# Performance work log

Hardware: AMD Instinct MI355X
Metric: run time of the kernel (lower is better)

The kernel has to match this reference:

```python
import jax, jax.numpy as jnp
import numpy as np


def setup_inputs() -> dict:
    key = jax.random.key(0)
    k1, k2, k3, k4, k5 = jax.random.split(key, 5)
    B, ENS, XDIM, YDIM = 8, 256, 8192, 256
    return {
        "Ens_ten": jax.random.normal(k1, (B, ENS, XDIM), dtype=jnp.float32),
        "H": jax.random.normal(k2, (XDIM, YDIM), dtype=jnp.float32),
        "y_true_mean": jax.random.normal(k3, (1, YDIM), dtype=jnp.float32),
        "y_true_std": jax.random.normal(k4, (1, YDIM), dtype=jnp.float32),
        "noise": jax.random.normal(k5, (B, YDIM, ENS), dtype=jnp.float32),
    }


def reference(Ens_ten, H, y_true_mean, y_true_std, noise):
    # Ens_ten: [b, ens, xdim]; H: [xdim, ydim]
    b, ens, xdim = Ens_ten.shape
    Y = jnp.einsum('bex,xy->bey', Ens_ten, H)          # observation_func (linear)
    x_m = jnp.mean(Ens_ten, axis=1, keepdims=True)     # [b,1,xdim]
    y_m = jnp.mean(Y, axis=1, keepdims=True)           # [b,1,ydim]
    Xc = jnp.swapaxes(Ens_ten - x_m, 1, 2)             # [b,xdim,ens]
    Yc = jnp.swapaxes(Y - y_m, 1, 2)                   # [b,ydim,ens]
    C_xy = jnp.einsum('bxe,bye->bxy', Xc, Yc) / ens    # [b,xdim,ydim]
    C_yy = jnp.einsum('bue,bve->buv', Yc, Yc) / ens    # [b,ydim,ydim]
    R = jnp.diag(jnp.square(y_true_std)[0])            # [ydim,ydim], broadcasts over batch
    A = R + C_yy                                       # [b,ydim,ydim]
    # torch.linalg.solve(A, C_xy, left=False): K = C_xy @ inv(A)
    K = jnp.swapaxes(
        jnp.linalg.solve(jnp.swapaxes(A, 1, 2), jnp.swapaxes(C_xy, 1, 2)), 1, 2
    )                                                  # [b,xdim,ydim]
    R_2 = noise * jnp.square(y_true_std)[:, :, None]   # [b,ydim,ens]
    innov = y_true_mean[:, :, None] - Yc + R_2         # [b,ydim,ens]
    update = jnp.einsum('bxy,bye->bxe', K, innov)      # [b,xdim,ens]
    return Ens_ten + jnp.swapaxes(update, 1, 2)
```

## Files before the change

### kernel.cpp

```cpp
#include <hip/hip_runtime.h>

#define ENSN 256
#define XDIM 8192
#define YD 256
#define BATCH 8

#define OFF_Y   0
#define OFF_YC  524288
#define OFF_AUG 1048576
#define OFF_W   2097152
#define OFF_XM  2621440

typedef __attribute__((ext_vector_type(4))) short short4v;
typedef __attribute__((ext_vector_type(8))) short short8v;
typedef __attribute__((ext_vector_type(4))) float float4v;

__device__ __forceinline__ unsigned short f2bf_rne(float x) {
    unsigned u = __float_as_uint(x);
    u += 0x7FFFu + ((u >> 16) & 1u);
    return (unsigned short)(u >> 16);
}

__global__ __launch_bounds__(256) void k1_colmean(const float* __restrict__ E,
                                                  float* __restrict__ xm) {
    int x = blockIdx.x * 256 + threadIdx.x;
    int b = blockIdx.y;
    const float* p = E + (size_t)b * ENSN * XDIM + x;
    float s = 0.f;
    #pragma unroll 8
    for (int e = 0; e < ENSN; e++) s += p[(size_t)e * XDIM];
    xm[b * XDIM + x] = s * (1.0f / ENSN);
}

__global__ __launch_bounds__(256) void kc_h(const float* __restrict__ H,
                                            short* __restrict__ Hthi,
                                            short* __restrict__ Htlo) {
    __shared__ float T[64][65];
    int k0 = blockIdx.x * 64, n0 = blockIdx.y * 64;
    int tid = threadIdx.x;
    int c = tid & 63, g = tid >> 6;
    #pragma unroll
    for (int p = 0; p < 16; p++)
        T[g + p * 4][c] = H[(size_t)(k0 + g + p * 4) * YD + n0 + c];
    __syncthreads();
    #pragma unroll
    for (int p = 0; p < 16; p++) {
        int nn = g + p * 4;
        float v = T[c][nn];
        unsigned short h = f2bf_rne(v);
        float hf = __uint_as_float(((unsigned)h) << 16);
        unsigned short l2 = f2bf_rne(v - hf);
        Hthi[(size_t)(n0 + nn) * XDIM + k0 + c] = (short)h;
        Htlo[(size_t)(n0 + nn) * XDIM + k0 + c] = (short)l2;
    }
}

#define EST 40
#define BST 40

__global__ __launch_bounds__(512, 2) void k2m_ygemm(const float* __restrict__ E,
                                                    const short* __restrict__ Hthi,
                                                    const short* __restrict__ Htlo,
                                                    float* __restrict__ Y) {
    __shared__ __align__(16) short Ehi[64 * EST];
    __shared__ __align__(16) short Elo[64 * EST];
    __shared__ __align__(16) short Bhi[256 * BST];
    __shared__ __align__(16) short Blo[256 * BST];
    int tid = threadIdx.x;
    int lane = tid & 63;
    int w = tid >> 6;
    int m0 = blockIdx.x * 64;
    int kb0 = blockIdx.y * 512;
    int wr = (w & 1) * 32;
    int wc = (w >> 1) * 64;
    float4v acc[8];
    #pragma unroll
    for (int i = 0; i < 8; i++) acc[i] = (float4v){0.f, 0.f, 0.f, 0.f};

    int erow = tid >> 3, ecol = (tid & 7) * 4;
    int brow = tid >> 1, bhalf = (tid & 1) * 16;
    int fr = lane & 15, fg = lane >> 4;

    for (int s = 0; s < 16; s++) {
        int kb = kb0 + s * 32;
        float4 ev = *(const float4*)&E[(size_t)(m0 + erow) * XDIM + kb + ecol];
        float vv[4] = {ev.x, ev.y, ev.z, ev.w};
        short4v hi4, lo4;
        #pragma unroll
        for (int j = 0; j < 4; j++) {
            unsigned short h = f2bf_rne(vv[j]);
            float hf = __uint_as_float(((unsigned)h) << 16);
            unsigned short l2 = f2bf_rne(vv[j] - hf);
            hi4[j] = (short)h; lo4[j] = (short)l2;
        }
        *(short4v*)&Ehi[erow * EST + ecol] = hi4;
        *(short4v*)&Elo[erow * EST + ecol] = lo4;
        short8v bh0 = *(const short8v*)&Hthi[(size_t)brow * XDIM + kb + bhalf];
        short8v bh1 = *(const short8v*)&Hthi[(size_t)brow * XDIM + kb + bhalf + 8];
        short8v bl0 = *(const short8v*)&Htlo[(size_t)brow * XDIM + kb + bhalf];
        short8v bl1 = *(const short8v*)&Htlo[(size_t)brow * XDIM + kb + bhalf + 8];
        *(short8v*)&Bhi[brow * BST + bhalf]     = bh0;
        *(short8v*)&Bhi[brow * BST + bhalf + 8] = bh1;
        *(short8v*)&Blo[brow * BST + bhalf]     = bl0;
        *(short8v*)&Blo[brow * BST + bhalf + 8] = bl1;
        __syncthreads();
        short8v ah[2], al[2], bhf[4], blf[4];
        #pragma unroll
        for (int ti = 0; ti < 2; ti++) {
            ah[ti] = *(const short8v*)&Ehi[(wr + ti * 16 + fr) * EST + fg * 8];
            al[ti] = *(const short8v*)&Elo[(wr + ti * 16 + fr) * EST + fg * 8];
        }
        #pragma unroll
        for (int tj = 0; tj < 4; tj++) {
            bhf[tj] = *(const short8v*)&Bhi[(wc + tj * 16 + fr) * BST + fg * 8];
            blf[tj] = *(const short8v*)&Blo[(wc + tj * 16 + fr) * BST + fg * 8];
        }
        #pragma unroll
        for (int ti = 0; ti < 2; ti++)
            #pragma unroll
            for (int tj = 0; tj < 4; tj++) {
                int a = ti * 4 + tj;
                acc[a] = __builtin_amdgcn_mfma_f32_16x16x32_bf16(ah[ti], bhf[tj], acc[a], 0, 0, 0);
                acc[a] = __builtin_amdgcn_mfma_f32_16x16x32_bf16(ah[ti], blf[tj], acc[a], 0, 0, 0);
                acc[a] = __builtin_amdgcn_mfma_f32_16x16x32_bf16(al[ti], bhf[tj], acc[a], 0, 0, 0);
            }
        __syncthreads();
    }
    #pragma unroll
    for (int ti = 0; ti < 2; ti++)
        #pragma unroll
        for (int tj = 0; tj < 4; tj++)
            #pragma unroll
            for (int q = 0; q < 4; q++) {
                int row = m0 + wr + ti * 16 + fg * 4 + q;
                int col = wc + tj * 16 + fr;
                atomicAdd(&Y[row * YD + col], acc[ti * 4 + tj][q]);
            }
}

__global__ __launch_bounds__(256) void k3_center(const float* __restrict__ Y,
                                                 const float* __restrict__ ytm,
                                                 const float* __restrict__ ystd,
                                                 const float* __restrict__ noise,
                                                 float* __restrict__ Yc,
                                                 float* __restrict__ aug) {
    int b = blockIdx.y, tid = threadIdx.x;
    int y0 = blockIdx.x * 64;
    __shared__ float red[4][64];
    __shared__ float ym[64], tms[64], s2[64];
    __shared__ float T[64][65];
    int yl = tid & 63, q = tid >> 6;
    float s = 0.f;
    for (int e = q * 64; e < q * 64 + 64; e++)
        s += Y[(size_t)(b * ENSN + e) * YD + y0 + yl];
    red[q][yl] = s;
    __syncthreads();
    if (tid < 64) {
        ym[tid] = (red[0][tid] + red[1][tid] + red[2][tid] + red[3][tid]) * (1.0f / ENSN);
        float sd = ystd[y0 + tid];
        s2[tid] = sd * sd;
        tms[tid] = ytm[y0 + tid];
    }
    __syncthreads();
    for (int e0 = 0; e0 < ENSN; e0 += 64) {
        #pragma unroll
        for (int p = 0; p < 16; p++) {
            int er = q + p * 4;
            T[er][yl] = Y[(size_t)(b * ENSN + e0 + er) * YD + y0 + yl];
        }
        __syncthreads();
        int ec = yl;
        #pragma unroll
        for (int p = 0; p < 16; p++) {
            int yr = q + p * 4;
            int y = y0 + yr, e = e0 + ec;
            float yv = T[ec][yr] - ym[yr];
            Yc[(size_t)b * YD * ENSN + (size_t)y * ENSN + e] = yv;
            aug[(size_t)b * YD * 512 + (size_t)y * 512 + 256 + e] =
                tms[yr] - yv + noise[(size_t)b * YD * ENSN + (size_t)y * ENSN + e] * s2[yr];
        }
        __syncthreads();
    }
}

__global__ __launch_bounds__(256) void k4_cyy(const float* __restrict__ Yc,
                                              const float* __restrict__ ystd,
                                              float* __restrict__ aug) {
    __shared__ float As[16][68];
    __shared__ float Bs[16][68];
    int tid = threadIdx.x;
    int m0 = blockIdx.x * 64, n0 = blockIdx.y * 64, b = blockIdx.z;
    const float* Ycb = Yc + (size_t)b * YD * ENSN;
    int tr = tid >> 4, tc = tid & 15;
    float acc[4][4];
    #pragma unroll
    for (int i = 0; i < 4; i++)
        #pragma unroll
        for (int j = 0; j < 4; j++) acc[i][j] = 0.f;
    int al = tid & 15, am0 = tid >> 4;
    for (int k0 = 0; k0 < ENSN; k0 += 16) {
        #pragma unroll
        for (int p = 0; p < 4; p++) {
            int am = am0 + p * 16;
            As[al][am] = Ycb[(m0 + am) * ENSN + k0 + al];
            Bs[al][am] = Ycb[(n0 + am) * ENSN + k0 + al];
        }
        __syncthreads();
        #pragma unroll
        for (int kk = 0; kk < 16; kk++) {
            float4 a = *(const float4*)&As[kk][tr * 4];
            float4 bb = *(const float4*)&Bs[kk][tc * 4];
            float af[4] = {a.x, a.y, a.z, a.w};
            float bf[4] = {bb.x, bb.y, bb.z, bb.w};
            #pragma unroll
            for (int i = 0; i < 4; i++)
                #pragma unroll
                for (int j = 0; j < 4; j++) acc[i][j] += af[i] * bf[j];
        }
        __syncthreads();
    }
    float* augb = aug + (size_t)b * YD * 512;
    #pragma unroll
    for (int i = 0; i < 4; i++) {
        int u = m0 + tr * 4 + i;
        #pragma unroll
        for (int j = 0; j < 4; j++) {
            int v = n0 + tc * 4 + j;
            float val = acc[i][j] * (1.0f / ENSN);
            if (u == v) { float sv = ystd[u]; val += sv * sv; }
            augb[u * 512 + v] = val;
        }
    }
}

#define RSTP 484
#define LSTP 233

__global__ __launch_bounds__(1024, 4) void k5p_panel(float* __restrict__ aug, int c0) {
    __shared__ __align__(16) float R[32 * RSTP];
    __shared__ float Ls[32 * LSTP];
    __shared__ __align__(16) float Dg[32 * 33];
    __shared__ float invd[32];
    int b = blockIdx.x, tid = threadIdx.x;
    float* A = aug + (size_t)b * 256 * 512;
    int r5 = tid >> 5, c5 = tid & 31;
    int WR = 480 - c0;
    int W2 = 224 - c0;

    Dg[r5 * 33 + c5] = A[(c0 + r5) * 512 + c0 + c5];
    __syncthreads();
    if (tid < 32) {
        float u[32];
        #pragma unroll
        for (int c = 0; c < 32; c++) u[c] = Dg[tid * 33 + c];
        for (int j = 0; j < 31; j++) {
            float pv = __shfl(u[j], j);
            float f = u[j] / pv;
            #pragma unroll
            for (int c = 0; c < 32; c++) {
                if (c > j) {
                    float ujc = __shfl(u[c], j);
                    if (tid > j) u[c] -= f * ujc;
                }
            }
            if (tid > j) u[j] = f;
        }
        #pragma unroll
        for (int c = 0; c < 32; c++) Dg[tid * 33 + c] = u[c];
        invd[tid] = 1.0f / u[tid];
    }
    for (int cc = c5; cc < WR; cc += 32)
        R[r5 * RSTP + cc] = A[(c0 + r5) * 512 + c0 + 32 + cc];
    for (int row = r5; row < W2; row += 32)
        Ls[c5 * LSTP + row] = A[(c0 + 32 + row) * 512 + c0 + c5];
    __syncthreads();
    A[(c0 + r5) * 512 + c0 + c5] = Dg[r5 * 33 + c5];
    if (tid < WR) {
        float y[32];
        #pragma unroll
        for (int j = 0; j < 32; j++) {
            float s = R[j * RSTP + tid];
            #pragma unroll
            for (int m = 0; m < 32; m++)
                if (m < j) s -= Dg[j * 33 + m] * y[m];
            y[j] = s;
        }
        #pragma unroll
        for (int j = 0; j < 32; j++)
            A[(c0 + j) * 512 + c0 + 32 + tid] = y[j];
    }
    if (tid >= 512 && tid < 512 + W2) {
        int row = tid - 512;
        float l[32];
        #pragma unroll
        for (int j = 0; j < 32; j++) {
            float s = Ls[j * LSTP + row];
            #pragma unroll
            for (int m = 0; m < 32; m++)
                if (m < j) s -= l[m] * Dg[m * 33 + j];
            l[j] = s * invd[j];
        }
        #pragma unroll
        for (int j = 0; j < 32; j++)
            Ls[j * LSTP + row] = l[j];
    }
    __syncthreads();
    for (int row = r5; row < W2; row += 32)
        A[(c0 + 32 + row) * 512 + c0 + c5] = Ls[c5 * LSTP + row];
}

__global__ __launch_bounds__(256) void k5t_trail(float* __restrict__ aug, int c0) {
    __shared__ __align__(16) float Lt[32][36];
    __shared__ __align__(16) float Ut[32][36];
    int b = blockIdx.z, tid = threadIdx.x;
    float* A = aug + (size_t)b * 256 * 512;
    int r0  = c0 + 32 + blockIdx.x * 32;
    int cc0 = c0 + 32 + blockIdx.y * 32;
    int lr = tid >> 3, lc = (tid & 7) * 4;
    *(float4*)&Lt[lr][lc] = *(const float4*)&A[(size_t)(r0 + lr) * 512 + c0 + lc];
    *(float4*)&Ut[lr][lc] = *(const float4*)&A[(size_t)(c0 + lr) * 512 + cc0 + lc];
    __syncthreads();
    float* gp = &A[(size_t)(r0 + lr) * 512 + cc0 + lc];
    float4 acc = *(const float4*)gp;
    #pragma unroll
    for (int k = 0; k < 32; k++) {
        float lv = Lt[lr][k];
        float4 uv = *(const float4*)&Ut[k][lc];
        acc.x -= lv * uv.x;
        acc.y -= lv * uv.y;
        acc.z -= lv * uv.z;
        acc.w -= lv * uv.w;
    }
    *(float4*)gp = acc;
}

__global__ __launch_bounds__(64) void k5i_invu(const float* __restrict__ aug,
                                               float* __restrict__ invU) {
    __shared__ float Dg[32 * 33];
    __shared__ float invd[32];
    int p = blockIdx.x, b = blockIdx.y, tid = threadIdx.x;
    const float* A = aug + (size_t)b * 256 * 512;
    int c0 = 32 * p;
    for (int i = tid; i < 1024; i += 64)
        Dg[(i >> 5) * 33 + (i & 31)] = A[(size_t)(c0 + (i >> 5)) * 512 + c0 + (i & 31)];
    __syncthreads();
    if (tid < 32) invd[tid] = 1.0f / Dg[tid * 33 + tid];
    __syncthreads();
    if (tid < 32) {
        int c = tid;
        float x[32];
        #pragma unroll
        for (int j = 31; j >= 0; j--) {
            float s = (j == c) ? 1.0f : 0.0f;
            #pragma unroll
            for (int m = 0; m < 32; m++)
                if (m > j) s -= Dg[j * 33 + m] * x[m];
            x[j] = s * invd[j];
        }
        float* op = invU + (size_t)(b * 8 + p) * 1024;
        #pragma unroll
        for (int j = 0; j < 32; j++) op[j * 32 + c] = x[j];
    }
}

#define ZST  68
#define LBST 36

__global__ __launch_bounds__(512, 2) void k5s_solve(float* __restrict__ aug,
                                                    const float* __restrict__ invU) {
    __shared__ __align__(16) float Zs[256 * ZST];
    __shared__ __align__(16) float Lb[224 * LBST];
    __shared__ __align__(16) float Dg[32 * 33];
    int b = blockIdx.y, tid = threadIdx.x;
    float* A = aug + (size_t)b * 256 * 512;
    int cb = blockIdx.x * 64;
    int c = tid & 63, g = tid >> 6;
    int rr = tid >> 5, cc = tid & 31;

    for (int r = g; r < 256; r += 8)
        Zs[r * ZST + c] = A[r * 512 + 256 + cb + c];

    for (int p = 7; p >= 0; p--) {
        int c0 = 32 * p, na = c0;
        for (int i = tid; i < 1024; i += 512)
            Dg[(i >> 5) * 33 + (i & 31)] = invU[(size_t)(b * 8 + p) * 1024 + i];
        for (int r = rr; r < na; r += 16)
            Lb[r * LBST + cc] = A[r * 512 + c0 + cc];
        __syncthreads();
        float z[32];
        #pragma unroll
        for (int m = 0; m < 32; m++) z[m] = Zs[(c0 + m) * ZST + c];
        float xr[4];
        #pragma unroll
        for (int r4 = 0; r4 < 4; r4++) {
            const float* dr = &Dg[(g * 4 + r4) * 33];
            float s0 = 0.f, s1 = 0.f, s2 = 0.f, s3 = 0.f;
            #pragma unroll
            for (int m = 0; m < 32; m += 4) {
                s0 += dr[m + 0] * z[m + 0];
                s1 += dr[m + 1] * z[m + 1];
                s2 += dr[m + 2] * z[m + 2];
                s3 += dr[m + 3] * z[m + 3];
            }
            xr[r4] = (s0 + s1) + (s2 + s3);
        }
        __syncthreads();
        #pragma unroll
        for (int r4 = 0; r4 < 4; r4++)
            Zs[(c0 + g * 4 + r4) * ZST + c] = xr[r4];
        __syncthreads();
        if (na > 0) {
            float zx[32];
            #pragma unroll
            for (int k = 0; k < 32; k++) zx[k] = Zs[(c0 + k) * ZST + c];
            for (int r = g; r < na; r += 8) {
                const float* lp = &Lb[r * LBST];
                float a0 = 0.f, a1 = 0.f, a2 = 0.f, a3 = 0.f;
                #pragma unroll
                for (int k = 0; k < 32; k += 4) {
                    float4 lv = *(const float4*)(lp + k);
                    a0 += lv.x * zx[k + 0];
                    a1 += lv.y * zx[k + 1];
                    a2 += lv.z * zx[k + 2];
                    a3 += lv.w * zx[k + 3];
                }
                Zs[r * ZST + c] -= (a0 + a1) + (a2 + a3);
            }
        }
        __syncthreads();
    }

    for (int r = g; r < 256; r += 8)
        A[r * 512 + 256 + cb + c] = Zs[r * ZST + c];
}

__global__ __launch_bounds__(256) void k6_w(const float* __restrict__ Yc,
                                            const float* __restrict__ aug,
                                            float* __restrict__ W) {
    __shared__ float As[16][68];
    __shared__ float Bs[16][68];
    int tid = threadIdx.x;
    int m0 = blockIdx.x * 64, n0 = blockIdx.y * 64, b = blockIdx.z;
    const float* Ycb = Yc + (size_t)b * YD * ENSN;
    const float* augb = aug + (size_t)b * YD * 512;
    int tr = tid >> 4, tc = tid & 15;
    float acc[4][4];
    #pragma unroll
    for (int i = 0; i < 4; i++)
        #pragma unroll
        for (int j = 0; j < 4; j++) acc[i][j] = 0.f;
    int c = tid & 63, kr0 = tid >> 6;
    for (int k0 = 0; k0 < YD; k0 += 16) {
        #pragma unroll
        for (int p = 0; p < 4; p++) {
            int kk = kr0 + p * 4;
            As[kk][c] = Ycb[(k0 + kk) * ENSN + m0 + c];
            Bs[kk][c] = augb[(k0 + kk) * 512 + 256 + n0 + c];
        }
        __syncthreads();
        #pragma unroll
        for (int kk = 0; kk < 16; kk++) {
            float4 a = *(const float4*)&As[kk][tr * 4];
            float4 bb = *(const float4*)&Bs[kk][tc * 4];
            float af[4] = {a.x, a.y, a.z, a.w};
            float bf[4] = {bb.x, bb.y, bb.z, bb.w};
            #pragma unroll
            for (int i = 0; i < 4; i++)
                #pragma unroll
                for (int j = 0; j < 4; j++) acc[i][j] += af[i] * bf[j];
        }
        __syncthreads();
    }
    float* Wb = W + (size_t)b * ENSN * ENSN;
    #pragma unroll
    for (int i = 0; i < 4; i++)
        #pragma unroll
        for (int j = 0; j < 4; j++)
            Wb[(m0 + tr * 4 + i) * ENSN + n0 + tc * 4 + j] = acc[i][j] * (1.0f / ENSN);
}

__global__ __launch_bounds__(256) void kw_w(const float* __restrict__ W,
                                            short* __restrict__ Wthi,
                                            short* __restrict__ Wtlo) {
    __shared__ float T[64][65];
    int f0 = blockIdx.x * 64, e0 = blockIdx.y * 64, b = blockIdx.z;
    const float* Wb = W + (size_t)b * ENSN * ENSN;
    int tid = threadIdx.x;
    int c = tid & 63, g = tid >> 6;
    #pragma unroll
    for (int p = 0; p < 16; p++)
        T[g + p * 4][c] = Wb[(size_t)(f0 + g + p * 4) * ENSN + e0 + c];
    __syncthreads();
    #pragma unroll
    for (int p = 0; p < 16; p++) {
        int ee = g + p * 4;
        float v = T[c][ee];
        unsigned short h = f2bf_rne(v);
        float hf = __uint_as_float(((unsigned)h) << 16);
        unsigned short l2 = f2bf_rne(v - hf);
        size_t o = (size_t)b * ENSN * ENSN + (size_t)(e0 + ee) * ENSN + f0 + c;
        Wthi[o] = (short)h;
        Wtlo[o] = (short)l2;
    }
}

#define WST 36
#define XST 36

__global__ __launch_bounds__(512, 2) void k7m_update(const float* __restrict__ E,
                                                     const short* __restrict__ Wthi,
                                                     const short* __restrict__ Wtlo,
                                                     const float* __restrict__ xm,
                                                     float* __restrict__ out) {
    __shared__ __align__(16) short Ahi[256 * WST];
    __shared__ __align__(16) short Alo[256 * WST];
    __shared__ __align__(16) short Bhi[64 * XST];
    __shared__ __align__(16) short Blo[64 * XST];
    __shared__ float xs[64];
    int tid = threadIdx.x;
    int lane = tid & 63;
    int w = tid >> 6;
    int x0 = blockIdx.x * 64;
    int b = blockIdx.y;
    const short* Whb = Wthi + (size_t)b * ENSN * ENSN;
    const short* Wlb = Wtlo + (size_t)b * ENSN * ENSN;
    const float* Eb = E + (size_t)b * ENSN * XDIM;
    if (tid < 64) xs[tid] = xm[b * XDIM + x0 + tid];
    __syncthreads();
    int wr = (w & 3) * 64;
    int wc = (w >> 2) * 32;
    float4v acc[8];
    #pragma unroll
    for (int i = 0; i < 8; i++) acc[i] = (float4v){0.f, 0.f, 0.f, 0.f};
    int fr = lane & 15, fg = lane >> 4;
    int ae = tid >> 2, ach = (tid & 3) * 8;
    int bx = tid & 63, bkq = tid >> 6;

    for (int s = 0; s < 8; s++) {
        int k0 = s * 32;
        #pragma unroll
        for (int h = 0; h < 2; h++) {
            int e = ae + h * 128;
            *(short8v*)&Ahi[e * WST + ach] = *(const short8v*)&Whb[(size_t)e * ENSN + k0 + ach];
            *(short8v*)&Alo[e * WST + ach] = *(const short8v*)&Wlb[(size_t)e * ENSN + k0 + ach];
        }
        short4v hi4, lo4;
        #pragma unroll
        for (int j = 0; j < 4; j++) {
            float v = Eb[(size_t)(k0 + bkq * 4 + j) * XDIM + x0 + bx] - xs[bx];
            unsigned short h = f2bf_rne(v);
            float hf = __uint_as_float(((unsigned)h) << 16);
            unsigned short l2 = f2bf_rne(v - hf);
            hi4[j] = (short)h; lo4[j] = (short)l2;
        }
        *(short4v*)&Bhi[bx * XST + bkq * 4] = hi4;
        *(short4v*)&Blo[bx * XST + bkq * 4] = lo4;
        __syncthreads();
        short8v ah[4], al[4], bhf[2], blf[2];
        #pragma unroll
        for (int ti = 0; ti < 4; ti++) {
            ah[ti] = *(const short8v*)&Ahi[(wr + ti * 16 + fr) * WST + fg * 8];
            al[ti] = *(const short8v*)&Alo[(wr + ti * 16 + fr) * WST + fg * 8];
        }
        #pragma unroll
        for (int tj = 0; tj < 2; tj++) {
            bhf[tj] = *(const short8v*)&Bhi[(wc + tj * 16 + fr) * XST + fg * 8];
            blf[tj] = *(const short8v*)&Blo[(wc + tj * 16 + fr) * XST + fg * 8];
        }
        #pragma unroll
        for (int ti = 0; ti < 4; ti++)
            #pragma unroll
            for (int tj = 0; tj < 2; tj++) {
                int a = ti * 2 + tj;
                acc[a] = __builtin_amdgcn_mfma_f32_16x16x32_bf16(ah[ti], bhf[tj], acc[a], 0, 0, 0);
                acc[a] = __builtin_amdgcn_mfma_f32_16x16x32_bf16(ah[ti], blf[tj], acc[a], 0, 0, 0);
                acc[a] = __builtin_amdgcn_mfma_f32_16x16x32_bf16(al[ti], bhf[tj], acc[a], 0, 0, 0);
            }
        __syncthreads();
    }
    #pragma unroll
    for (int ti = 0; ti < 4; ti++)
        #pragma unroll
        for (int tj = 0; tj < 2; tj++)
            #pragma unroll
            for (int q = 0; q < 4; q++) {
                int e = wr + ti * 16 + fg * 4 + q;
                int x = x0 + wc + tj * 16 + fr;
                size_t idx = (size_t)(b * ENSN + e) * XDIM + x;
                out[idx] = E[idx] + acc[ti * 2 + tj][q];
            }
}

extern "C" void kernel_launch(void* const* d_in, const int* in_sizes, int n_in,
                              void* d_out, int out_size, void* d_ws, size_t ws_size,
                              hipStream_t stream) {
    const float* Ens   = (const float*)d_in[0];
    const float* H     = (const float*)d_in[1];
    const float* ytm   = (const float*)d_in[2];
    const float* ystd  = (const float*)d_in[3];
    const float* noise = (const float*)d_in[4];
    float* out = (float*)d_out;
    float* ws  = (float*)d_ws;

    float* Y   = ws + OFF_Y;
    float* Yc  = ws + OFF_YC;
    float* aug = ws + OFF_AUG;
    float* W   = ws + OFF_W;
    float* xm  = ws + OFF_XM;
    short* Hthi = (short*)(ws + 524288);
    short* Htlo = (short*)(ws + 1572864);
    short* Wthi = (short*)(ws + 0);
    short* Wtlo = (short*)(ws + 262144);
    float* invU = ws + OFF_W;

    hipMemsetAsync(Y, 0, (size_t)2048 * 256 * sizeof(float), stream);

    k1_colmean<<<dim3(XDIM / 256, BATCH), 256, 0, stream>>>(Ens, xm);
    kc_h<<<dim3(XDIM / 64, YD / 64), 256, 0, stream>>>(H, Hthi, Htlo);
    k2m_ygemm<<<dim3(2048 / 64, 16), 512, 0, stream>>>(Ens, Hthi, Htlo, Y);
    k3_center<<<dim3(4, BATCH), 256, 0, stream>>>(Y, ytm, ystd, noise, Yc, aug);
    k4_cyy<<<dim3(4, 4, BATCH), 256, 0, stream>>>(Yc, ystd, aug);
    for (int p = 0; p < 8; p++) {
        k5p_panel<<<dim3(BATCH), 1024, 0, stream>>>(aug, 32 * p);
        if (p < 7)
            k5t_trail<<<dim3(7 - p, 15 - p, BATCH), 256, 0, stream>>>(aug, 32 * p);
    }
    k5i_invu<<<dim3(8, BATCH), 64, 0, stream>>>(aug, invU);
    k5s_solve<<<dim3(4, BATCH), 512, 0, stream>>>(aug, invU);
    k6_w<<<dim3(4, 4, BATCH), 256, 0, stream>>>(Yc, aug, W);
    kw_w<<<dim3(4, 4, BATCH), 256, 0, stream>>>(W, Wthi, Wtlo);
    k7m_update<<<dim3(XDIM / 64, BATCH), 512, 0, stream>>>(Ens, Wthi, Wtlo, xm, out);
}
```

Baseline: 658.8 us.

## Invert panel diagonal blocks inside LU panel kernel and widen solve grid

The panel kernel now explicitly inverts the 32x32 unit-lower and upper diagonal factors. It then applies those inverses as small dense mat-vecs instead of running serial triangular substitutions for the U row-block and L column-block. The inverse of U is written to global memory there, which removes the separate k5i_invu launch. k5s_solve is retiled to 32 columns per block, doubling its grid to get more parallelism, at the cost of extra shared memory in the panel kernel and a serial inversion step on two warps.

```diff
diff --git a/kernel.cpp b/kernel.cpp
--- a/kernel.cpp
+++ b/kernel.cpp
@@ -236,10 +236,13 @@
 #define RSTP 484
 #define LSTP 233
 
-__global__ __launch_bounds__(1024, 4) void k5p_panel(float* __restrict__ aug, int c0) {
+__global__ __launch_bounds__(1024, 4) void k5p_panel(float* __restrict__ aug,
+                                                     float* __restrict__ invU, int c0) {
     __shared__ __align__(16) float R[32 * RSTP];
     __shared__ float Ls[32 * LSTP];
     __shared__ __align__(16) float Dg[32 * 33];
+    __shared__ float iL[32 * 33];
+    __shared__ float iU[32 * 33];
     __shared__ float invd[32];
     int b = blockIdx.x, tid = threadIdx.x;
     float* A = aug + (size_t)b * 256 * 512;
@@ -275,30 +278,72 @@
         Ls[c5 * LSTP + row] = A[(c0 + 32 + row) * 512 + c0 + c5];
     __syncthreads();
     A[(c0 + r5) * 512 + c0 + c5] = Dg[r5 * 33 + c5];
+    if (tid < 32) {
+        int c = tid;
+        float x[32];
+        #pragma unroll
+        for (int j = 0; j < 32; j++) {
+            float s = (j == c) ? 1.0f : 0.0f;
+            #pragma unroll
+            for (int m = 0; m < 32; m++)
+                if (m < j) s -= Dg[j * 33 + m] * x[m];
+            x[j] = s;
+        }
+        #pragma unroll
+        for (int j = 0; j < 32; j++) iL[j * 33 + c] = x[j];
+    } else if (tid < 64) {
+        int c = tid - 32;
+        float x[32];
+        #pragma unroll
+        for (int j = 31; j >= 0; j--) {
+            float s = (j == c) ? 1.0f : 0.0f;
+            #pragma unroll
+            for (int m = 0; m < 32; m++)
+                if (m > j) s -= Dg[j * 33 + m] * x[m];
+            x[j] = s * invd[j];
+        }
+        #pragma unroll
+        for (int j = 0; j < 32; j++) iU[j * 33 + c] = x[j];
+        float* op = invU + (size_t)(b * 8 + (c0 >> 5)) * 1024;
+        #pragma unroll
+        for (int j = 0; j < 32; j++) op[j * 32 + c] = x[j];
+    }
+    __syncthreads();
     if (tid < WR) {
-        float y[32];
+        float rv[32];
+        #pragma unroll
+        for (int m = 0; m < 32; m++) rv[m] = R[m * RSTP + tid];
         #pragma unroll
         for (int j = 0; j < 32; j++) {
-            float s = R[j * RSTP + tid];
-            #pragma unroll
-            for (int m = 0; m < 32; m++)
-                if (m < j) s -= Dg[j * 33 + m] * y[m];
-            y[j] = s;
-        }
-        #pragma unroll
-        for (int j = 0; j < 32; j++)
-            A[(c0 + j) * 512 + c0 + 32 + tid] = y[j];
+            const float* lj = &iL[j * 33];
+            float s0 = 0.f, s1 = 0.f, s2 = 0.f, s3 = 0.f;
+            #pragma unroll
+            for (int m = 0; m < 32; m += 4) {
+                s0 += lj[m + 0] * rv[m + 0];
+                s1 += lj[m + 1] * rv[m + 1];
+                s2 += lj[m + 2] * rv[m + 2];
+                s3 += lj[m + 3] * rv[m + 3];
+            }
+            A[(c0 + j) * 512 + c0 + 32 + tid] = (s0 + s1) + (s2 + s3);
+        }
     }
     if (tid >= 512 && tid < 512 + W2) {
         int row = tid - 512;
+        float av[32];
+        #pragma unroll
+        for (int m = 0; m < 32; m++) av[m] = Ls[m * LSTP + row];
         float l[32];
         #pragma unroll
         for (int j = 0; j < 32; j++) {
-            float s = Ls[j * LSTP + row];
-            #pragma unroll
-            for (int m = 0; m < 32; m++)
-                if (m < j) s -= l[m] * Dg[m * 33 + j];
-            l[j] = s * invd[j];
+            float s0 = 0.f, s1 = 0.f, s2 = 0.f, s3 = 0.f;
+            #pragma unroll
+            for (int m = 0; m < 32; m += 4) {
+                s0 += av[m + 0] * iU[(m + 0) * 33 + j];
+                s1 += av[m + 1] * iU[(m + 1) * 33 + j];
+                s2 += av[m + 2] * iU[(m + 2) * 33 + j];
+                s3 += av[m + 3] * iU[(m + 3) * 33 + j];
+            }
+            l[j] = (s0 + s1) + (s2 + s3);
         }
         #pragma unroll
         for (int j = 0; j < 32; j++)
@@ -334,36 +379,7 @@
     *(float4*)gp = acc;
 }
 
-__global__ __launch_bounds__(64) void k5i_invu(const float* __restrict__ aug,
-                                               float* __restrict__ invU) {
-    __shared__ float Dg[32 * 33];
-    __shared__ float invd[32];
-    int p = blockIdx.x, b = blockIdx.y, tid = threadIdx.x;
-    const float* A = aug + (size_t)b * 256 * 512;
-    int c0 = 32 * p;
-    for (int i = tid; i < 1024; i += 64)
-        Dg[(i >> 5) * 33 + (i & 31)] = A[(size_t)(c0 + (i >> 5)) * 512 + c0 + (i & 31)];
-    __syncthreads();
-    if (tid < 32) invd[tid] = 1.0f / Dg[tid * 33 + tid];
-    __syncthreads();
-    if (tid < 32) {
-        int c = tid;
-        float x[32];
-        #pragma unroll
-        for (int j = 31; j >= 0; j--) {
-            float s = (j == c) ? 1.0f : 0.0f;
-            #pragma unroll
-            for (int m = 0; m < 32; m++)
-                if (m > j) s -= Dg[j * 33 + m] * x[m];
-            x[j] = s * invd[j];
-        }
-        float* op = invU + (size_t)(b * 8 + p) * 1024;
-        #pragma unroll
-        for (int j = 0; j < 32; j++) op[j * 32 + c] = x[j];
-    }
-}
-
-#define ZST  68
+#define ZST  36
 #define LBST 36
 
 __global__ __launch_bounds__(512, 2) void k5s_solve(float* __restrict__ aug,
@@ -373,11 +389,11 @@
     __shared__ __align__(16) float Dg[32 * 33];
     int b = blockIdx.y, tid = threadIdx.x;
     float* A = aug + (size_t)b * 256 * 512;
-    int cb = blockIdx.x * 64;
-    int c = tid & 63, g = tid >> 6;
+    int cb = blockIdx.x * 32;
+    int c = tid & 31, g = tid >> 5;
     int rr = tid >> 5, cc = tid & 31;
 
-    for (int r = g; r < 256; r += 8)
+    for (int r = g; r < 256; r += 16)
         Zs[r * ZST + c] = A[r * 512 + 256 + cb + c];
 
     for (int p = 7; p >= 0; p--) {
@@ -390,10 +406,10 @@
         float z[32];
         #pragma unroll
         for (int m = 0; m < 32; m++) z[m] = Zs[(c0 + m) * ZST + c];
-        float xr[4];
-        #pragma unroll
-        for (int r4 = 0; r4 < 4; r4++) {
-            const float* dr = &Dg[(g * 4 + r4) * 33];
+        float xr[2];
+        #pragma unroll
+        for (int r2 = 0; r2 < 2; r2++) {
+            const float* dr = &Dg[(g * 2 + r2) * 33];
             float s0 = 0.f, s1 = 0.f, s2 = 0.f, s3 = 0.f;
             #pragma unroll
             for (int m = 0; m < 32; m += 4) {
@@ -402,18 +418,18 @@
                 s2 += dr[m + 2] * z[m + 2];
                 s3 += dr[m + 3] * z[m + 3];
             }
-            xr[r4] = (s0 + s1) + (s2 + s3);
-        }
-        __syncthreads();
-        #pragma unroll
-        for (int r4 = 0; r4 < 4; r4++)
-            Zs[(c0 + g * 4 + r4) * ZST + c] = xr[r4];
+            xr[r2] = (s0 + s1) + (s2 + s3);
+        }
+        __syncthreads();
+        #pragma unroll
+        for (int r2 = 0; r2 < 2; r2++)
+            Zs[(c0 + g * 2 + r2) * ZST + c] = xr[r2];
         __syncthreads();
         if (na > 0) {
             float zx[32];
             #pragma unroll
             for (int k = 0; k < 32; k++) zx[k] = Zs[(c0 + k) * ZST + c];
-            for (int r = g; r < na; r += 8) {
+            for (int r = g; r < na; r += 16) {
                 const float* lp = &Lb[r * LBST];
                 float a0 = 0.f, a1 = 0.f, a2 = 0.f, a3 = 0.f;
                 #pragma unroll
@@ -430,7 +446,7 @@
         __syncthreads();
     }
 
-    for (int r = g; r < 256; r += 8)
+    for (int r = g; r < 256; r += 16)
         A[r * 512 + 256 + cb + c] = Zs[r * ZST + c];
 }
 
@@ -621,12 +637,11 @@
     k3_center<<<dim3(4, BATCH), 256, 0, stream>>>(Y, ytm, ystd, noise, Yc, aug);
     k4_cyy<<<dim3(4, 4, BATCH), 256, 0, stream>>>(Yc, ystd, aug);
     for (int p = 0; p < 8; p++) {
-        k5p_panel<<<dim3(BATCH), 1024, 0, stream>>>(aug, 32 * p);
+        k5p_panel<<<dim3(BATCH), 1024, 0, stream>>>(aug, invU, 32 * p);
         if (p < 7)
             k5t_trail<<<dim3(7 - p, 15 - p, BATCH), 256, 0, stream>>>(aug, 32 * p);
     }
-    k5i_invu<<<dim3(8, BATCH), 64, 0, stream>>>(aug, invU);
-    k5s_solve<<<dim3(4, BATCH), 512, 0, stream>>>(aug, invU);
+    k5s_solve<<<dim3(8, BATCH), 512, 0, stream>>>(aug, invU);
     k6_w<<<dim3(4, 4, BATCH), 256, 0, stream>>>(Yc, aug, W);
     kw_w<<<dim3(4, 4, BATCH), 256, 0, stream>>>(W, Wthi, Wtlo);
     k7m_update<<<dim3(XDIM / 64, BATCH), 512, 0, stream>>>(Ens, Wthi, Wtlo, xm, out);
```

New measurement: 728.9 us. 1.11x slower.
